# Optimization experiments

Hardware: AMD Instinct MI355X
Metric: run time of the kernel (lower is better)

## Reference

```python
import jax, jax.numpy as jnp
import numpy as np

HIDDEN = 1024
HEADS = 16
HEAD_DIM = HIDDEN // HEADS
SCALE = 1.0 / (HEAD_DIM ** 0.5)


def setup_inputs() -> dict:
    key = jax.random.key(0)
    k1, k2, k3 = jax.random.split(key, 3)
    B, S = 2, 2048
    x = jax.random.normal(k1, (B, S, HIDDEN), dtype=jnp.float32)
    # torch Linear weights: (out_features, in_features), y = x @ W.T
    qkv_w = jax.random.normal(k2, (3 * HIDDEN, HIDDEN), dtype=jnp.float32) * (HIDDEN ** -0.5)
    out_w = jax.random.normal(k3, (HIDDEN, HIDDEN), dtype=jnp.float32) * (HIDDEN ** -0.5)
    return {"x": x, "qkv_w": qkv_w, "out_w": out_w}


def reference(x, qkv_w, out_w):
    B, S, H = x.shape
    qkv = jnp.einsum('bsh,oh->bso', x, qkv_w)  # [B,S,3H]
    q, k, v = jnp.split(qkv, 3, axis=-1)
    def heads(t):
        return t.reshape(B, S, HEADS, HEAD_DIM).transpose(0, 2, 1, 3)  # [B,nh,S,hd]
    q, k, v = heads(q), heads(k), heads(v)
    scores = jnp.einsum('bhqd,bhkd->bhqk', q, k) * SCALE  # [B,nh,S,S]
    attn = jax.nn.softmax(scores, axis=-1)
    out = jnp.einsum('bhqk,bhkd->bhqd', attn, v)  # [B,nh,S,hd]
    out = out.transpose(0, 2, 1, 3).reshape(B, S, H)
    return jnp.einsum('bsh,oh->bso', out, out_w)
```

## Files before the change

### kernel.cpp

```cpp
#include <hip/hip_runtime.h>
#include <hip/hip_bf16.h>

#define BB 2
#define SS 2048
#define HH 1024
#define NH 16
#define HD 64
#define MM (BB * SS)
#define N_QKV (3 * HH)
#define KK HH

typedef __attribute__((ext_vector_type(8))) short short8;
typedef __attribute__((ext_vector_type(4))) float floatx4;
typedef __attribute__((ext_vector_type(16))) float floatx16;

#define MFMA16(a, b, c) __builtin_amdgcn_mfma_f32_16x16x32_bf16(a, b, c, 0, 0, 0)
#define MFMA32(a, b, c) __builtin_amdgcn_mfma_f32_32x32x16_bf16(a, b, c, 0, 0, 0)

__device__ __forceinline__ unsigned short f2bf(float f) {
  unsigned int u = __builtin_bit_cast(unsigned int, f);
  u += 0x7FFFu + ((u >> 16) & 1u);
  return (unsigned short)(u >> 16);
}

__device__ __forceinline__ float fexp2(float x) {
#if __has_builtin(__builtin_amdgcn_exp2f)
  return __builtin_amdgcn_exp2f(x);
#else
  float r; asm("v_exp_f32 %0, %1" : "=v"(r) : "v"(x)); return r;
#endif
}

__device__ __forceinline__ unsigned int pack2e(float lo, float hi) {
  unsigned int a = __builtin_bit_cast(unsigned int, lo) + 0x8000u;
  unsigned int b = __builtin_bit_cast(unsigned int, hi) + 0x8000u;
  return __builtin_amdgcn_perm(b, a, 0x07060302u);
}

__device__ __forceinline__ unsigned int cvtpk(float lo, float hi) {
  unsigned int r;
  asm("v_cvt_pk_bf16_f32 %0, %1, %2" : "=v"(r) : "v"(lo), "v"(hi));
  return r;
}

__device__ __forceinline__ uint4 cvt8pk(float4 lo, float4 hi) {
  uint4 u;
  u.x = cvtpk(lo.x, lo.y);
  u.y = cvtpk(lo.z, lo.w);
  u.z = cvtpk(hi.x, hi.y);
  u.w = cvtpk(hi.z, hi.w);
  return u;
}

__device__ __forceinline__ void gload_lds16(const void* g, void* l) {
  __builtin_amdgcn_global_load_lds((const __attribute__((address_space(1))) void*)g,
                                   (__attribute__((address_space(3))) void*)l,
                                   16, 0, 0);
}

__global__ __launch_bounds__(256) void cast_xw(const float* __restrict__ x,
                                               const float* __restrict__ w1,
                                               unsigned short* __restrict__ xb,
                                               unsigned short* __restrict__ w1b) {
  const int NX = MM * KK / 8;
  int i = blockIdx.x * 256 + threadIdx.x;
  const float* s; unsigned short* d; int o;
  if (i < NX) { s = x;  d = xb;  o = i; }
  else        { s = w1; d = w1b; o = i - NX; }
  float4 lo = *(const float4*)(s + (size_t)o * 8);
  float4 hi = *(const float4*)(s + (size_t)o * 8 + 4);
  *(uint4*)(d + (size_t)o * 8) = cvt8pk(lo, hi);
}

__global__ __launch_bounds__(256) void cast_g(const float* __restrict__ s,
                                              unsigned short* __restrict__ d) {
  size_t i = (size_t)blockIdx.x * 256 + threadIdx.x;
  float4 lo = *(const float4*)(s + i * 8);
  float4 hi = *(const float4*)(s + i * 8 + 4);
  *(uint4*)(d + i * 8) = cvt8pk(lo, hi);
}

__global__ __launch_bounds__(256) void gemm_qkv_dma(const unsigned short* __restrict__ Xb,
                                                    const unsigned short* __restrict__ Wb,
                                                    unsigned short* __restrict__ qb,
                                                    unsigned short* __restrict__ kb,
                                                    unsigned short* __restrict__ vtb) {
  __shared__ __attribute__((aligned(16))) unsigned short As[2][128 * 32];
  __shared__ __attribute__((aligned(16))) unsigned short Bs[2][128 * 32];
  const int tid = threadIdx.x;
  const int wave = tid >> 6;
  const int lane = tid & 63;
  const int quad = lane >> 4, lc = lane & 15;
  const int m0 = blockIdx.y * 128, n0 = blockIdx.x * 128;
  const int wm = (wave >> 1) * 64, wn = (wave & 1) * 64;
  const int sr = tid >> 2, sc = (tid & 3) * 8;

  floatx4 acc[4][4];
#pragma unroll
  for (int i = 0; i < 4; i++)
#pragma unroll
    for (int j = 0; j < 4; j++) acc[i][j] = (floatx4){0.f, 0.f, 0.f, 0.f};

  const unsigned short* Axp = Xb + (size_t)(m0 + sr) * KK + sc;
  const unsigned short* Bxp = Wb + (size_t)(n0 + sr) * KK + sc;

#define STAGEQ(buf, k0)                                               \
  do {                                                                \
    gload_lds16(Axp + (k0), &As[buf][wave * 512]);                    \
    gload_lds16(Axp + (size_t)64 * KK + (k0), &As[buf][wave * 512 + 2048]); \
    gload_lds16(Bxp + (k0), &Bs[buf][wave * 512]);                    \
    gload_lds16(Bxp + (size_t)64 * KK + (k0), &Bs[buf][wave * 512 + 2048]); \
  } while (0)

  STAGEQ(0, 0);

  const int NIT = KK / 32;
  for (int it = 0; it < NIT; ++it) {
    const int cb = it & 1;
    if (it + 1 < NIT) {
      STAGEQ(cb ^ 1, (it + 1) * 32);
      asm volatile("s_waitcnt vmcnt(4)" ::: "memory");
    } else {
      asm volatile("s_waitcnt vmcnt(0)" ::: "memory");
    }
    __builtin_amdgcn_s_barrier();
    __builtin_amdgcn_sched_barrier(0);
    short8 af[4], bfr[4];
#pragma unroll
    for (int i = 0; i < 4; i++) {
      af[i]  = *(const short8*)(&As[cb][(wm + i * 16 + lc) * 32 + quad * 8]);
      bfr[i] = *(const short8*)(&Bs[cb][(wn + i * 16 + lc) * 32 + quad * 8]);
    }
#pragma unroll
    for (int i = 0; i < 4; i++)
#pragma unroll
      for (int j = 0; j < 4; j++) acc[i][j] = MFMA16(af[i], bfr[j], acc[i][j]);
    __builtin_amdgcn_sched_barrier(0);
    __builtin_amdgcn_s_barrier();
  }
#undef STAGEQ

  const float QSCALE = 0.125f * 1.44269504f;
#pragma unroll
  for (int j = 0; j < 4; j++) {
    int n = n0 + wn + j * 16 + lc;
#pragma unroll
    for (int i = 0; i < 4; i++) {
      int mbase = m0 + wm + i * 16 + quad * 4;
      int b = mbase >> 11;
      int s0 = mbase & 2047;
      if (n < HH) {
        int h = n >> 6, d = n & 63;
#pragma unroll
        for (int r = 0; r < 4; r++)
          qb[(((size_t)(b * NH + h) * SS + s0 + r) * HD) + d] = f2bf(acc[i][j][r] * QSCALE);
      } else if (n < 2 * HH) {
        int n2 = n - HH; int h = n2 >> 6, d = n2 & 63;
#pragma unroll
        for (int r = 0; r < 4; r++)
          kb[(((size_t)(b * NH + h) * SS + s0 + r) * HD) + d] = f2bf(acc[i][j][r]);
      } else {
        int n2 = n - 2 * HH; int h = n2 >> 6, d = n2 & 63;
        ushort4 p;
        p.x = f2bf(acc[i][j][0]); p.y = f2bf(acc[i][j][1]);
        p.z = f2bf(acc[i][j][2]); p.w = f2bf(acc[i][j][3]);
        *(ushort4*)(vtb + ((size_t)(b * NH + h) * HD + d) * SS + s0) = p;
      }
    }
  }
}

__global__ __launch_bounds__(256) void gemm_qkv_f32(const unsigned short* __restrict__ Xb,
                                                    const float* __restrict__ Wf,
                                                    unsigned short* __restrict__ qb,
                                                    unsigned short* __restrict__ kb,
                                                    unsigned short* __restrict__ vtb) {
  __shared__ __attribute__((aligned(16))) unsigned short As[128 * 32];
  __shared__ __attribute__((aligned(16))) unsigned short Bs[128 * 32];
  const int tid = threadIdx.x;
  const int wave = tid >> 6, lane = tid & 63;
  const int quad = lane >> 4, lc = lane & 15;
  const int m0 = blockIdx.y * 128, n0 = blockIdx.x * 128;
  const int wm = (wave >> 1) * 64, wn = (wave & 1) * 64;
  const int sr = tid >> 2, sc = (tid & 3) * 8;

  floatx4 acc[4][4];
#pragma unroll
  for (int i = 0; i < 4; i++)
#pragma unroll
    for (int j = 0; j < 4; j++) acc[i][j] = (floatx4){0.f, 0.f, 0.f, 0.f};

  const unsigned short* Axp = Xb + (size_t)(m0 + sr) * KK + sc;
  unsigned short* AsD = As + wave * 512;
  const float* Bg = Wf + (size_t)(n0 + sr) * KK + sc;
  unsigned short* BsW = Bs + wave * 512 + lane * 8;
  float4 b0l = *(const float4*)(Bg),                    b0h = *(const float4*)(Bg + 4);
  float4 b1l = *(const float4*)(Bg + (size_t)64 * KK),  b1h = *(const float4*)(Bg + (size_t)64 * KK + 4);

  for (int it = 0; it < KK / 32; ++it) {
    const int k0 = it * 32;
    __syncthreads();
    gload_lds16(Axp + k0, AsD);
    gload_lds16(Axp + (size_t)64 * KK + k0, AsD + 2048);
    *(uint4*)(BsW) = cvt8pk(b0l, b0h);
    *(uint4*)(BsW + 2048) = cvt8pk(b1l, b1h);
    if (it + 1 < KK / 32) {
      b0l = *(const float4*)(Bg + k0 + 32);                    b0h = *(const float4*)(Bg + k0 + 36);
      b1l = *(const float4*)(Bg + k0 + 32 + (size_t)64 * KK);  b1h = *(const float4*)(Bg + k0 + 36 + (size_t)64 * KK);
    }
    __syncthreads();
    short8 af[4], bfr[4];
#pragma unroll
    for (int i = 0; i < 4; i++) {
      af[i]  = *(const short8*)(As + (wm + i * 16 + lc) * 32 + quad * 8);
      bfr[i] = *(const short8*)(Bs + (wn + i * 16 + lc) * 32 + quad * 8);
    }
#pragma unroll
    for (int i = 0; i < 4; i++)
#pragma unroll
      for (int j = 0; j < 4; j++) acc[i][j] = MFMA16(af[i], bfr[j], acc[i][j]);
  }

  const float QSCALE = 0.125f * 1.44269504f;
#pragma unroll
  for (int j = 0; j < 4; j++) {
    int n = n0 + wn + j * 16 + lc;
#pragma unroll
    for (int i = 0; i < 4; i++) {
      int mbase = m0 + wm + i * 16 + quad * 4;
      int b = mbase >> 11;
      int s0 = mbase & 2047;
      if (n < HH) {
        int h = n >> 6, d = n & 63;
#pragma unroll
        for (int r = 0; r < 4; r++)
          qb[(((size_t)(b * NH + h) * SS + s0 + r) * HD) + d] = f2bf(acc[i][j][r] * QSCALE);
      } else if (n < 2 * HH) {
        int n2 = n - HH; int h = n2 >> 6, d = n2 & 63;
#pragma unroll
        for (int r = 0; r < 4; r++)
          kb[(((size_t)(b * NH + h) * SS + s0 + r) * HD) + d] = f2bf(acc[i][j][r]);
      } else {
        int n2 = n - 2 * HH; int h = n2 >> 6, d = n2 & 63;
        ushort4 p;
        p.x = f2bf(acc[i][j][0]); p.y = f2bf(acc[i][j][1]);
        p.z = f2bf(acc[i][j][2]); p.w = f2bf(acc[i][j][3]);
        *(ushort4*)(vtb + ((size_t)(b * NH + h) * HD + d) * SS + s0) = p;
      }
    }
  }
}

__device__ __forceinline__ int co(int row, int c16) {
  return row * 64 + ((c16 ^ ((row ^ (row >> 3)) & 7)) << 3);
}

__global__ __launch_bounds__(256, 2) void attn_kernel(const unsigned short* __restrict__ qg,
                                                      const unsigned short* __restrict__ kg,
                                                      const unsigned short* __restrict__ vtg,
                                                      unsigned short* __restrict__ og) {
  __shared__ __attribute__((aligned(16))) unsigned short Sall[16384];
  unsigned short* Qs = Sall;
  unsigned short* Ks = Sall + 8192;
  unsigned short* Vs = Sall + 12288;

  const int tid = threadIdx.x;
  const int w = tid >> 6, lane = tid & 63;
  const int hl = lane >> 5, c = lane & 31;
  const int q0 = blockIdx.x * 128;
  const int head = blockIdx.y, b = blockIdx.z;

  const unsigned short* qbase = qg + (size_t)(b * NH + head) * SS * HD;
  const unsigned short* kbase = kg + (size_t)(b * NH + head) * SS * HD;
  const unsigned short* vbase = vtg + (size_t)(b * NH + head) * HD * SS;

  {
    int row = tid >> 3, cc = tid & 7;
#pragma unroll
    for (int s = 0; s < 4; s++)
      *(uint4*)(Qs + co(row + 32 * s, cc)) =
          *(const uint4*)(qbase + (size_t)(q0 + row + 32 * s) * HD + cc * 8);
  }

  const int frow = tid >> 3, fc = tid & 7;
  uint4 k0r = *(const uint4*)(kbase + (size_t)frow * HD + fc * 8);
  uint4 k1r = *(const uint4*)(kbase + (size_t)(frow + 32) * HD + fc * 8);
  uint4 v0r = *(const uint4*)(vbase + (size_t)frow * SS + fc * 8);
  uint4 v1r = *(const uint4*)(vbase + (size_t)(frow + 32) * SS + fc * 8);

  floatx16 oacc0, oacc1, lacc;
#pragma unroll
  for (int i = 0; i < 16; i++) { oacc0[i] = 0.f; oacc1[i] = 0.f; lacc[i] = 0.f; }

  short8 ones;
#pragma unroll
  for (int i = 0; i < 8; i++) ones[i] = (short)0x3F80;

  short8 qa[4];

  for (int kt = 0; kt < SS; kt += 64) {
    __syncthreads();
    *(uint4*)(Ks + co(frow, fc)) = k0r;
    *(uint4*)(Ks + co(frow + 32, fc)) = k1r;
    *(uint4*)(Vs + co(frow, fc)) = v0r;
    *(uint4*)(Vs + co(frow + 32, fc)) = v1r;
    if (kt + 64 < SS) {
      k0r = *(const uint4*)(kbase + (size_t)(kt + 64 + frow) * HD + fc * 8);
      k1r = *(const uint4*)(kbase + (size_t)(kt + 96 + frow) * HD + fc * 8);
      v0r = *(const uint4*)(vbase + (size_t)frow * SS + kt + 64 + fc * 8);
      v1r = *(const uint4*)(vbase + (size_t)(frow + 32) * SS + kt + 64 + fc * 8);
    }
    __syncthreads();

    if (kt == 0) {
#pragma unroll
      for (int ks = 0; ks < 4; ks++)
        qa[ks] = *(const short8*)(Qs + co(w * 32 + c, ks * 2 + hl));
    }

    floatx16 sacc0, sacc1;
#pragma unroll
    for (int i = 0; i < 16; i++) { sacc0[i] = 0.f; sacc1[i] = 0.f; }
#pragma unroll
    for (int ks = 0; ks < 4; ks++) {
      short8 ka0 = *(const short8*)(Ks + co(c, ks * 2 + hl));
      short8 ka1 = *(const short8*)(Ks + co(32 + c, ks * 2 + hl));
      sacc0 = MFMA32(ka0, qa[ks], sacc0);
      sacc1 = MFMA32(ka1, qa[ks], sacc1);
    }

    short8 pb[4];
#pragma unroll
    for (int kb = 0; kb < 4; kb++) {
      const floatx16& s = (kb < 2) ? sacc0 : sacc1;
      int base = (kb & 1) * 8;
      unsigned int u0 = pack2e(fexp2(s[base + 0]), fexp2(s[base + 1]));
      unsigned int u1 = pack2e(fexp2(s[base + 2]), fexp2(s[base + 3]));
      unsigned int u2 = pack2e(fexp2(s[base + 4]), fexp2(s[base + 5]));
      unsigned int u3 = pack2e(fexp2(s[base + 6]), fexp2(s[base + 7]));
      uint4 u = {u0, u1, u2, u3};
      pb[kb] = __builtin_bit_cast(short8, u);
    }

#pragma unroll
    for (int kb = 0; kb < 4; kb++) {
      uint2 lo0 = *(const uint2*)(Vs + co(c, 2 * kb) + 4 * hl);
      uint2 hi0 = *(const uint2*)(Vs + co(c, 2 * kb + 1) + 4 * hl);
      uint4 a0 = {lo0.x, lo0.y, hi0.x, hi0.y};
      short8 va0 = __builtin_bit_cast(short8, a0);
      uint2 lo1 = *(const uint2*)(Vs + co(32 + c, 2 * kb) + 4 * hl);
      uint2 hi1 = *(const uint2*)(Vs + co(32 + c, 2 * kb + 1) + 4 * hl);
      uint4 a1 = {lo1.x, lo1.y, hi1.x, hi1.y};
      short8 va1 = __builtin_bit_cast(short8, a1);
      oacc0 = MFMA32(va0, pb[kb], oacc0);
      oacc1 = MFMA32(va1, pb[kb], oacc1);
      lacc = MFMA32(ones, pb[kb], lacc);
    }
  }

  __syncthreads();
  unsigned short* sc = Sall + w * 2176;
  float inv = 1.0f / lacc[0];
#pragma unroll
  for (int t = 0; t < 8; t++) {
    int d0 = ((2 * t) & 3) + 8 * (t >> 1) + 4 * hl;
    *(unsigned int*)(sc + c * 68 + d0) = pack2e(oacc0[2 * t] * inv, oacc0[2 * t + 1] * inv);
    *(unsigned int*)(sc + c * 68 + 32 + d0) = pack2e(oacc1[2 * t] * inv, oacc1[2 * t + 1] * inv);
  }
  {
    int ql = lane >> 1, hf = lane & 1;
    size_t row = (size_t)(b * SS + q0 + w * 32 + ql);
    unsigned short* dst = og + row * HH + head * 64 + hf * 32;
    const unsigned short* srcp = sc + ql * 68 + hf * 32;
#pragma unroll
    for (int s = 0; s < 4; s++) {
      uint2 a = *(const uint2*)(srcp + s * 8);
      uint2 bq = *(const uint2*)(srcp + s * 8 + 4);
      uint4 v = {a.x, a.y, bq.x, bq.y};
      *(uint4*)(dst + s * 8) = v;
    }
  }
}

__global__ __launch_bounds__(256) void gemm_out_dma(const unsigned short* __restrict__ A,
                                                    const unsigned short* __restrict__ Wb,
                                                    float* __restrict__ C) {
  __shared__ __attribute__((aligned(16))) unsigned short As[2][128 * 32];
  __shared__ __attribute__((aligned(16))) unsigned short Bs[2][64 * 32];
  const int tid = threadIdx.x;
  const int wave = tid >> 6, lane = tid & 63;
  const int quad = lane >> 4, lc = lane & 15;
  const int m0 = blockIdx.y * 128, n0 = blockIdx.x * 64;
  const int wm = (wave >> 1) * 64, wn = (wave & 1) * 32;
  const int sr = tid >> 2, sc = (tid & 3) * 8;

  floatx4 acc[4][2];
#pragma unroll
  for (int i = 0; i < 4; i++)
#pragma unroll
    for (int j = 0; j < 2; j++) acc[i][j] = (floatx4){0.f, 0.f, 0.f, 0.f};

  const unsigned short* Axp = A + (size_t)(m0 + sr) * KK + sc;
  const unsigned short* Bxp = Wb + (size_t)(n0 + sr) * KK + sc;

#define STAGEO(buf, k0)                                               \
  do {                                                                \
    gload_lds16(Axp + (k0), &As[buf][wave * 512]);                    \
    gload_lds16(Axp + (size_t)64 * KK + (k0), &As[buf][wave * 512 + 2048]); \
    gload_lds16(Bxp + (k0), &Bs[buf][wave * 512]);                    \
  } while (0)

  STAGEO(0, 0);

  const int NIT = KK / 32;
  for (int it = 0; it < NIT; ++it) {
    const int cb = it & 1;
    if (it + 1 < NIT) {
      STAGEO(cb ^ 1, (it + 1) * 32);
      asm volatile("s_waitcnt vmcnt(3)" ::: "memory");
    } else {
      asm volatile("s_waitcnt vmcnt(0)" ::: "memory");
    }
    __builtin_amdgcn_s_barrier();
    __builtin_amdgcn_sched_barrier(0);
    short8 af[4], bfr[2];
#pragma unroll
    for (int i = 0; i < 4; i++)
      af[i] = *(const short8*)(&As[cb][(wm + i * 16 + lc) * 32 + quad * 8]);
#pragma unroll
    for (int j = 0; j < 2; j++)
      bfr[j] = *(const short8*)(&Bs[cb][(wn + j * 16 + lc) * 32 + quad * 8]);
#pragma unroll
    for (int i = 0; i < 4; i++)
#pragma unroll
      for (int j = 0; j < 2; j++) acc[i][j] = MFMA16(af[i], bfr[j], acc[i][j]);
    __builtin_amdgcn_sched_barrier(0);
    __builtin_amdgcn_s_barrier();
  }
#undef STAGEO

#pragma unroll
  for (int i = 0; i < 4; i++)
#pragma unroll
    for (int j = 0; j < 2; j++) {
      int m = m0 + wm + i * 16 + quad * 4;
      int n = n0 + wn + j * 16 + lc;
#pragma unroll
      for (int r = 0; r < 4; r++) C[(size_t)(m + r) * HH + n] = acc[i][j][r];
    }
}

extern "C" void kernel_launch(void* const* d_in, const int* in_sizes, int n_in,
                              void* d_out, int out_size, void* d_ws, size_t ws_size,
                              hipStream_t stream) {
  const float* x = (const float*)d_in[0];
  const float* qkv_w = (const float*)d_in[1];
  const float* out_w = (const float*)d_in[2];
  float* out = (float*)d_out;

  char* ws = (char*)d_ws;
  unsigned short* qb  = (unsigned short*)(ws + 0);
  unsigned short* kb  = (unsigned short*)(ws + 8388608);
  unsigned short* vtb = (unsigned short*)(ws + 16777216);
  unsigned short* xb  = (unsigned short*)(ws + 25165824);
  unsigned short* ao  = xb;
  unsigned short* wob = qb;

  const bool big = ws_size >= 40ull * 1024 * 1024;
  unsigned short* w1b = big ? (unsigned short*)(ws + 33554432) : nullptr;

  if (big) {
    cast_xw<<<dim3((MM * KK + N_QKV * KK) / 2048), dim3(256), 0, stream>>>(x, qkv_w, xb, w1b);
    gemm_qkv_dma<<<dim3(N_QKV / 128, MM / 128), dim3(256), 0, stream>>>(xb, w1b, qb, kb, vtb);
  } else {
    cast_g<<<dim3(MM * KK / 2048), dim3(256), 0, stream>>>(x, xb);
    gemm_qkv_f32<<<dim3(N_QKV / 128, MM / 128), dim3(256), 0, stream>>>(xb, qkv_w, qb, kb, vtb);
  }
  attn_kernel<<<dim3(SS / 128, NH, BB), dim3(256), 0, stream>>>(qb, kb, vtb, ao);
  cast_g<<<dim3(HH * KK / 2048), dim3(256), 0, stream>>>(out_w, wob);
  gemm_out_dma<<<dim3(HH / 64, MM / 128), dim3(256), 0, stream>>>(ao, wob, out);
}
```

Baseline: 192.6 us.

## Widen GEMM K-tiles to 64 with XOR swizzle, remap blocks, raise MFMA priority

Both bf16 GEMMs now stage 64-wide K tiles into LDS with an XOR-swizzled chunk layout, which halves the number of loop iterations and barriers and is meant to avoid LDS bank conflicts. Blocks are remapped from a 1D grid so that work is spread across XCDs. s_setprio is raised around the MFMA sections in the GEMMs and the attention kernel. The out_w cast is folded into the single initial cast kernel, which removes one launch. LDS use doubles, which may lower occupancy.

```diff
diff --git a/kernel.cpp b/kernel.cpp
--- a/kernel.cpp
+++ b/kernel.cpp
@@ -58,15 +58,19 @@
                                    16, 0, 0);
 }
 
-__global__ __launch_bounds__(256) void cast_xw(const float* __restrict__ x,
-                                               const float* __restrict__ w1,
-                                               unsigned short* __restrict__ xb,
-                                               unsigned short* __restrict__ w1b) {
+__global__ __launch_bounds__(256) void cast_all(const float* __restrict__ x,
+                                                const float* __restrict__ w1,
+                                                const float* __restrict__ w2,
+                                                unsigned short* __restrict__ xb,
+                                                unsigned short* __restrict__ w1b,
+                                                unsigned short* __restrict__ w2b) {
   const int NX = MM * KK / 8;
+  const int NW1 = N_QKV * KK / 8;
   int i = blockIdx.x * 256 + threadIdx.x;
   const float* s; unsigned short* d; int o;
-  if (i < NX) { s = x;  d = xb;  o = i; }
-  else        { s = w1; d = w1b; o = i - NX; }
+  if (i < NX)            { s = x;  d = xb;  o = i; }
+  else if (i < NX + NW1) { s = w1; d = w1b; o = i - NX; }
+  else                   { s = w2; d = w2b; o = i - (NX + NW1); }
   float4 lo = *(const float4*)(s + (size_t)o * 8);
   float4 hi = *(const float4*)(s + (size_t)o * 8 + 4);
   *(uint4*)(d + (size_t)o * 8) = cvt8pk(lo, hi);
@@ -85,15 +89,14 @@
                                                     unsigned short* __restrict__ qb,
                                                     unsigned short* __restrict__ kb,
                                                     unsigned short* __restrict__ vtb) {
-  __shared__ __attribute__((aligned(16))) unsigned short As[2][128 * 32];
-  __shared__ __attribute__((aligned(16))) unsigned short Bs[2][128 * 32];
+  __shared__ __attribute__((aligned(16))) unsigned short As[2][128 * 64];
+  __shared__ __attribute__((aligned(16))) unsigned short Bs[2][128 * 64];
   const int tid = threadIdx.x;
-  const int wave = tid >> 6;
-  const int lane = tid & 63;
+  const int wave = tid >> 6, lane = tid & 63;
   const int quad = lane >> 4, lc = lane & 15;
-  const int m0 = blockIdx.y * 128, n0 = blockIdx.x * 128;
+  const int wg = (blockIdx.x & 7) * 96 + (blockIdx.x >> 3);
+  const int m0 = (wg / 24) * 128, n0 = (wg % 24) * 128;
   const int wm = (wave >> 1) * 64, wn = (wave & 1) * 64;
-  const int sr = tid >> 2, sc = (tid & 3) * 8;
 
   floatx4 acc[4][4];
 #pragma unroll
@@ -101,40 +104,49 @@
 #pragma unroll
     for (int j = 0; j < 4; j++) acc[i][j] = (floatx4){0.f, 0.f, 0.f, 0.f};
 
-  const unsigned short* Axp = Xb + (size_t)(m0 + sr) * KK + sc;
-  const unsigned short* Bxp = Wb + (size_t)(n0 + sr) * KK + sc;
-
-#define STAGEQ(buf, k0)                                               \
-  do {                                                                \
-    gload_lds16(Axp + (k0), &As[buf][wave * 512]);                    \
-    gload_lds16(Axp + (size_t)64 * KK + (k0), &As[buf][wave * 512 + 2048]); \
-    gload_lds16(Bxp + (k0), &Bs[buf][wave * 512]);                    \
-    gload_lds16(Bxp + (size_t)64 * KK + (k0), &Bs[buf][wave * 512 + 2048]); \
+  const int srow = lane >> 3;
+  const int schk = (lane & 7) ^ srow;
+  const unsigned short* Ab = Xb + (size_t)(m0 + wave * 8 + srow) * KK + schk * 8;
+  const unsigned short* Bb = Wb + (size_t)(n0 + wave * 8 + srow) * KK + schk * 8;
+
+#define STAGEQ(buf, k0)                                                          \
+  do {                                                                           \
+    _Pragma("unroll")                                                            \
+    for (int g = 0; g < 4; g++) {                                                \
+      gload_lds16(Ab + (size_t)g * 32 * KK + (k0), &As[buf][(g * 32 + wave * 8) * 64]); \
+      gload_lds16(Bb + (size_t)g * 32 * KK + (k0), &Bs[buf][(g * 32 + wave * 8) * 64]); \
+    }                                                                            \
   } while (0)
 
   STAGEQ(0, 0);
 
-  const int NIT = KK / 32;
+  const int NIT = KK / 64;
   for (int it = 0; it < NIT; ++it) {
     const int cb = it & 1;
     if (it + 1 < NIT) {
-      STAGEQ(cb ^ 1, (it + 1) * 32);
-      asm volatile("s_waitcnt vmcnt(4)" ::: "memory");
+      STAGEQ(cb ^ 1, (it + 1) * 64);
+      asm volatile("s_waitcnt vmcnt(8)" ::: "memory");
     } else {
       asm volatile("s_waitcnt vmcnt(0)" ::: "memory");
     }
     __builtin_amdgcn_s_barrier();
     __builtin_amdgcn_sched_barrier(0);
-    short8 af[4], bfr[4];
-#pragma unroll
-    for (int i = 0; i < 4; i++) {
-      af[i]  = *(const short8*)(&As[cb][(wm + i * 16 + lc) * 32 + quad * 8]);
-      bfr[i] = *(const short8*)(&Bs[cb][(wn + i * 16 + lc) * 32 + quad * 8]);
-    }
-#pragma unroll
-    for (int i = 0; i < 4; i++)
-#pragma unroll
-      for (int j = 0; j < 4; j++) acc[i][j] = MFMA16(af[i], bfr[j], acc[i][j]);
+    __builtin_amdgcn_s_setprio(1);
+#pragma unroll
+    for (int kk = 0; kk < 2; kk++) {
+      short8 af[4], bfr[4];
+#pragma unroll
+      for (int i = 0; i < 4; i++) {
+        const int cs = ((kk * 4 + quad) ^ (lc & 7)) << 3;
+        af[i]  = *(const short8*)(&As[cb][(wm + i * 16 + lc) * 64 + cs]);
+        bfr[i] = *(const short8*)(&Bs[cb][(wn + i * 16 + lc) * 64 + cs]);
+      }
+#pragma unroll
+      for (int i = 0; i < 4; i++)
+#pragma unroll
+        for (int j = 0; j < 4; j++) acc[i][j] = MFMA16(af[i], bfr[j], acc[i][j]);
+    }
+    __builtin_amdgcn_s_setprio(0);
     __builtin_amdgcn_sched_barrier(0);
     __builtin_amdgcn_s_barrier();
   }
@@ -321,6 +333,7 @@
     floatx16 sacc0, sacc1;
 #pragma unroll
     for (int i = 0; i < 16; i++) { sacc0[i] = 0.f; sacc1[i] = 0.f; }
+    __builtin_amdgcn_s_setprio(1);
 #pragma unroll
     for (int ks = 0; ks < 4; ks++) {
       short8 ka0 = *(const short8*)(Ks + co(c, ks * 2 + hl));
@@ -328,6 +341,7 @@
       sacc0 = MFMA32(ka0, qa[ks], sacc0);
       sacc1 = MFMA32(ka1, qa[ks], sacc1);
     }
+    __builtin_amdgcn_s_setprio(0);
 
     short8 pb[4];
 #pragma unroll
@@ -342,6 +356,7 @@
       pb[kb] = __builtin_bit_cast(short8, u);
     }
 
+    __builtin_amdgcn_s_setprio(1);
 #pragma unroll
     for (int kb = 0; kb < 4; kb++) {
       uint2 lo0 = *(const uint2*)(Vs + co(c, 2 * kb) + 4 * hl);
@@ -356,6 +371,7 @@
       oacc1 = MFMA32(va1, pb[kb], oacc1);
       lacc = MFMA32(ones, pb[kb], lacc);
     }
+    __builtin_amdgcn_s_setprio(0);
   }
 
   __syncthreads();
@@ -385,14 +401,14 @@
 __global__ __launch_bounds__(256) void gemm_out_dma(const unsigned short* __restrict__ A,
                                                     const unsigned short* __restrict__ Wb,
                                                     float* __restrict__ C) {
-  __shared__ __attribute__((aligned(16))) unsigned short As[2][128 * 32];
-  __shared__ __attribute__((aligned(16))) unsigned short Bs[2][64 * 32];
+  __shared__ __attribute__((aligned(16))) unsigned short As[2][128 * 64];
+  __shared__ __attribute__((aligned(16))) unsigned short Bs[2][64 * 64];
   const int tid = threadIdx.x;
   const int wave = tid >> 6, lane = tid & 63;
   const int quad = lane >> 4, lc = lane & 15;
-  const int m0 = blockIdx.y * 128, n0 = blockIdx.x * 64;
+  const int wg = (blockIdx.x & 7) * 64 + (blockIdx.x >> 3);
+  const int m0 = (wg / 16) * 128, n0 = (wg % 16) * 64;
   const int wm = (wave >> 1) * 64, wn = (wave & 1) * 32;
-  const int sr = tid >> 2, sc = (tid & 3) * 8;
 
   floatx4 acc[4][2];
 #pragma unroll
@@ -400,40 +416,50 @@
 #pragma unroll
     for (int j = 0; j < 2; j++) acc[i][j] = (floatx4){0.f, 0.f, 0.f, 0.f};
 
-  const unsigned short* Axp = A + (size_t)(m0 + sr) * KK + sc;
-  const unsigned short* Bxp = Wb + (size_t)(n0 + sr) * KK + sc;
-
-#define STAGEO(buf, k0)                                               \
-  do {                                                                \
-    gload_lds16(Axp + (k0), &As[buf][wave * 512]);                    \
-    gload_lds16(Axp + (size_t)64 * KK + (k0), &As[buf][wave * 512 + 2048]); \
-    gload_lds16(Bxp + (k0), &Bs[buf][wave * 512]);                    \
+  const int srow = lane >> 3;
+  const int schk = (lane & 7) ^ srow;
+  const unsigned short* Ab = A  + (size_t)(m0 + wave * 8 + srow) * KK + schk * 8;
+  const unsigned short* Bb = Wb + (size_t)(n0 + wave * 8 + srow) * KK + schk * 8;
+
+#define STAGEO(buf, k0)                                                          \
+  do {                                                                           \
+    _Pragma("unroll")                                                            \
+    for (int g = 0; g < 4; g++)                                                  \
+      gload_lds16(Ab + (size_t)g * 32 * KK + (k0), &As[buf][(g * 32 + wave * 8) * 64]); \
+    _Pragma("unroll")                                                            \
+    for (int g = 0; g < 2; g++)                                                  \
+      gload_lds16(Bb + (size_t)g * 32 * KK + (k0), &Bs[buf][(g * 32 + wave * 8) * 64]); \
   } while (0)
 
   STAGEO(0, 0);
 
-  const int NIT = KK / 32;
+  const int NIT = KK / 64;
   for (int it = 0; it < NIT; ++it) {
     const int cb = it & 1;
     if (it + 1 < NIT) {
-      STAGEO(cb ^ 1, (it + 1) * 32);
-      asm volatile("s_waitcnt vmcnt(3)" ::: "memory");
+      STAGEO(cb ^ 1, (it + 1) * 64);
+      asm volatile("s_waitcnt vmcnt(6)" ::: "memory");
     } else {
       asm volatile("s_waitcnt vmcnt(0)" ::: "memory");
     }
     __builtin_amdgcn_s_barrier();
     __builtin_amdgcn_sched_barrier(0);
-    short8 af[4], bfr[2];
-#pragma unroll
-    for (int i = 0; i < 4; i++)
-      af[i] = *(const short8*)(&As[cb][(wm + i * 16 + lc) * 32 + quad * 8]);
-#pragma unroll
-    for (int j = 0; j < 2; j++)
-      bfr[j] = *(const short8*)(&Bs[cb][(wn + j * 16 + lc) * 32 + quad * 8]);
-#pragma unroll
-    for (int i = 0; i < 4; i++)
-#pragma unroll
-      for (int j = 0; j < 2; j++) acc[i][j] = MFMA16(af[i], bfr[j], acc[i][j]);
+    __builtin_amdgcn_s_setprio(1);
+#pragma unroll
+    for (int kk = 0; kk < 2; kk++) {
+      short8 af[4], bfr[2];
+#pragma unroll
+      for (int i = 0; i < 4; i++)
+        af[i] = *(const short8*)(&As[cb][(wm + i * 16 + lc) * 64 + (((kk * 4 + quad) ^ (lc & 7)) << 3)]);
+#pragma unroll
+      for (int j = 0; j < 2; j++)
+        bfr[j] = *(const short8*)(&Bs[cb][(wn + j * 16 + lc) * 64 + (((kk * 4 + quad) ^ (lc & 7)) << 3)]);
+#pragma unroll
+      for (int i = 0; i < 4; i++)
+#pragma unroll
+        for (int j = 0; j < 2; j++) acc[i][j] = MFMA16(af[i], bfr[j], acc[i][j]);
+    }
+    __builtin_amdgcn_s_setprio(0);
     __builtin_amdgcn_sched_barrier(0);
     __builtin_amdgcn_s_barrier();
   }
@@ -464,19 +490,22 @@
   unsigned short* vtb = (unsigned short*)(ws + 16777216);
   unsigned short* xb  = (unsigned short*)(ws + 25165824);
   unsigned short* ao  = xb;
-  unsigned short* wob = qb;
 
   const bool big = ws_size >= 40ull * 1024 * 1024;
   unsigned short* w1b = big ? (unsigned short*)(ws + 33554432) : nullptr;
+  unsigned short* w2b = big ? (unsigned short*)(ws + 39845888) : nullptr;
 
   if (big) {
-    cast_xw<<<dim3((MM * KK + N_QKV * KK) / 2048), dim3(256), 0, stream>>>(x, qkv_w, xb, w1b);
-    gemm_qkv_dma<<<dim3(N_QKV / 128, MM / 128), dim3(256), 0, stream>>>(xb, w1b, qb, kb, vtb);
+    cast_all<<<dim3(4096), dim3(256), 0, stream>>>(x, qkv_w, out_w, xb, w1b, w2b);
+    gemm_qkv_dma<<<dim3(768), dim3(256), 0, stream>>>(xb, w1b, qb, kb, vtb);
+    attn_kernel<<<dim3(SS / 128, NH, BB), dim3(256), 0, stream>>>(qb, kb, vtb, ao);
+    gemm_out_dma<<<dim3(512), dim3(256), 0, stream>>>(ao, w2b, out);
   } else {
+    unsigned short* wob = qb;
     cast_g<<<dim3(MM * KK / 2048), dim3(256), 0, stream>>>(x, xb);
     gemm_qkv_f32<<<dim3(N_QKV / 128, MM / 128), dim3(256), 0, stream>>>(xb, qkv_w, qb, kb, vtb);
-  }
-  attn_kernel<<<dim3(SS / 128, NH, BB), dim3(256), 0, stream>>>(qb, kb, vtb, ao);
-  cast_g<<<dim3(HH * KK / 2048), dim3(256), 0, stream>>>(out_w, wob);
-  gemm_out_dma<<<dim3(HH / 64, MM / 128), dim3(256), 0, stream>>>(ao, wob, out);
-}
+    attn_kernel<<<dim3(SS / 128, NH, BB), dim3(256), 0, stream>>>(qb, kb, vtb, ao);
+    cast_g<<<dim3(HH * KK / 2048), dim3(256), 0, stream>>>(out_w, wob);
+    gemm_out_dma<<<dim3(512), dim3(256), 0, stream>>>(ao, wob, out);
+  }
+}
```

Result: faster. 182.1 us (-5.5%).
